# Performance work log

Measured on AMD Instinct MI355X. Metric: run time of the kernel, lower is better.

## Reference

```python
import jax, jax.numpy as jnp
import numpy as np

H = 2048       # hidden_size
NH = 16        # num_attention_heads
HN = H // NH   # per-head dim = 128
B = 2
S = 2048
ALPHA = 32.0   # cogview pb-relax alpha


def setup_inputs() -> dict:
    key = jax.random.key(0)
    k1, k2, k3 = jax.random.split(key, 3)
    hidden_states = jax.random.normal(k1, (B, S, H), dtype=jnp.float32)
    # causal lower-triangular float mask [1,1,s,s]
    ltor_mask = jnp.tril(jnp.ones((S, S), dtype=jnp.float32))[None, None]
    # fused QKV projection params (torch Linear: y = x @ W.T + b)
    lim_qkv = 1.0 / np.sqrt(H)
    W_qkv = jax.random.uniform(k2, (3 * H, H), jnp.float32, -lim_qkv, lim_qkv)
    b_qkv = jnp.zeros((3 * H,), jnp.float32)
    W_out = jax.random.uniform(k3, (H, H), jnp.float32, -lim_qkv, lim_qkv)
    b_out = jnp.zeros((H,), jnp.float32)
    return {"hidden_states": hidden_states, "ltor_mask": ltor_mask,
            "W_qkv": W_qkv, "b_qkv": b_qkv, "W_out": W_out, "b_out": b_out}


def reference(hidden_states, ltor_mask, W_qkv, b_qkv, W_out, b_out):
    b, s, h = hidden_states.shape
    # fused QKV projection: [b,s,3h]
    qkv = hidden_states @ W_qkv.T + b_qkv
    q, k, v = jnp.split(qkv, 3, axis=-1)
    # [b,s,h] -> [b,n,s,hn]
    def heads(t):
        return t.reshape(b, s, NH, HN).transpose(0, 2, 1, 3)
    q, k, v = heads(q), heads(k), heads(v)
    # cogview_pb_relax: scale query before matmul
    scores = jnp.einsum('bnqd,bnkd->bnqk', q / jnp.sqrt(jnp.float32(HN)), k)
    mask = ltor_mask[:, :, -scores.shape[-2]:]
    scores = scores * mask - 10000.0 * (1.0 - mask)
    # pb-relax max rescaling (max is detached)
    scaled = scores / ALPHA
    maxes = jax.lax.stop_gradient(jnp.max(scaled.reshape(b, NH, -1), axis=-1))
    scores = (scaled - maxes[:, :, None, None]) * ALPHA
    probs = jax.nn.softmax(scores, axis=-1)
    ctx = jnp.einsum('bnqk,bnkd->bnqd', probs, v)
    ctx = ctx.transpose(0, 2, 1, 3).reshape(b, s, h)
    out = ctx @ W_out.T + b_out
    return out
```

## Files before the change

kernel.cpp:

```cpp
#include <hip/hip_runtime.h>

typedef __bf16 bf16;
typedef bf16 bf16x4 __attribute__((ext_vector_type(4)));
typedef bf16 bf16x8 __attribute__((ext_vector_type(8)));
typedef float f32x4 __attribute__((ext_vector_type(4)));

#define Bb 2
#define Ss 2048
#define Hh 2048
#define NHh 16
#define HNd 128
#define H3 6144
#define Mm 4096
#define SCALE_QK 0.08838834764831843f

__device__ __forceinline__ void async_copy16(void* lds, const void* g) {
  __builtin_amdgcn_global_load_lds(
      (const __attribute__((address_space(1))) unsigned int*)g,
      (__attribute__((address_space(3))) unsigned int*)lds, 16, 0, 0);
}

__global__ __launch_bounds__(256) void cvt_kernel(const float* __restrict__ in,
                                                  bf16* __restrict__ out, int n) {
  int i = (blockIdx.x * 256 + threadIdx.x) * 4;
  if (i < n) {
    float4 v = *reinterpret_cast<const float4*>(in + i);
    bf16x4 o;
    o[0] = (bf16)v.x; o[1] = (bf16)v.y; o[2] = (bf16)v.z; o[3] = (bf16)v.w;
    *reinterpret_cast<bf16x4*>(out + i) = o;
  }
}

template <int QM, int QN, int NRD>
__device__ __forceinline__ void gemm_phase(
    const bf16* asb, const bf16* bsb, int lm, int lg, int wm, int wn,
    bf16x8 (&af)[4][2], bf16x8 (&bfr)[4][2]) {
  if (NRD & 2) {
#pragma unroll
    for (int mi = 0; mi < 4; ++mi)
#pragma unroll
      for (int kk = 0; kk < 2; ++kk) {
        const int row = wm * 128 + (QM * 4 + mi) * 16 + lm;
        af[mi][kk] = *reinterpret_cast<const bf16x8*>(
            (const char*)asb + row * 128 + ((kk * 64 + lg * 16) ^ ((lm & 7) << 4)));
      }
  }
  if (NRD & 1) {
#pragma unroll
    for (int nj = 0; nj < 2; ++nj)
#pragma unroll
      for (int kk = 0; kk < 2; ++kk) {
        const int row = wn * 64 + (QN * 2 + nj) * 16 + lm;
        bfr[QN * 2 + nj][kk] = *reinterpret_cast<const bf16x8*>(
            (const char*)bsb + row * 128 + ((kk * 64 + lg * 16) ^ ((lm & 7) << 4)));
      }
  }
}

template <int QM, int QN>
__device__ __forceinline__ void mfma_quad(const bf16x8 (&af)[4][2],
                                          const bf16x8 (&bfr)[4][2],
                                          f32x4 (&acc)[8][4]) {
#pragma unroll
  for (int kk = 0; kk < 2; ++kk)
#pragma unroll
    for (int mi = 0; mi < 4; ++mi)
#pragma unroll
      for (int nj = 0; nj < 2; ++nj)
        acc[QM * 4 + mi][QN * 2 + nj] = __builtin_amdgcn_mfma_f32_16x16x32_bf16(
            af[mi][kk], bfr[QN * 2 + nj][kk], acc[QM * 4 + mi][QN * 2 + nj], 0, 0, 0);
}

template <int OUT_F32>
__global__ __launch_bounds__(512, 2) void gemm256_kernel(
    const bf16* __restrict__ A, const bf16* __restrict__ Bw,
    const float* __restrict__ bias, void* __restrict__ Cout,
    int M, int N, int K) {
  __shared__ __align__(16) bf16 As[2][256 * 64];
  __shared__ __align__(16) bf16 Bs[2][256 * 64];

  const int tid = threadIdx.x;
  const int lane = tid & 63;
  const int w = tid >> 6;
  const int wm = w >> 2, wn = w & 3;
  const int lm = lane & 15, lg = lane >> 4;
  const int m0 = blockIdx.y * 256, n0 = blockIdx.x * 256;
  const int srow = lane >> 3;
  const int sslot = lane & 7;

  auto stage = [&](int b, int t) {
#pragma unroll
    for (int l = 0; l < 4; ++l) {
      const int r = l * 64 + w * 8 + srow;
      async_copy16(&As[b][l * 4096 + w * 512],
                   A + (size_t)(m0 + r) * K + t * 64 + (sslot ^ srow) * 8);
    }
#pragma unroll
    for (int l = 0; l < 4; ++l) {
      const int r = l * 64 + w * 8 + srow;
      async_copy16(&Bs[b][l * 4096 + w * 512],
                   Bw + (size_t)(n0 + r) * K + t * 64 + (sslot ^ srow) * 8);
    }
  };

  f32x4 acc[8][4] = {};
  bf16x8 af[4][2], bfr[4][2];

#define PHASE(BS, QM, QN, NRD, ST, VM)                                         \
  do {                                                                         \
    gemm_phase<QM, QN, NRD>(&As[BS][0], &Bs[BS][0], lm, lg, wm, wn, af, bfr);  \
    if ((ST) >= 0) stage((BS), (ST));                                          \
    __builtin_amdgcn_s_barrier();                                              \
    __builtin_amdgcn_s_setprio(1);                                             \
    mfma_quad<QM, QN>(af, bfr, acc);                                           \
    __builtin_amdgcn_s_setprio(0);                                             \
    if ((VM) == 8) asm volatile("s_waitcnt vmcnt(8)" ::: "memory");            \
    else if ((VM) == 0) asm volatile("s_waitcnt vmcnt(0)" ::: "memory");       \
    __builtin_amdgcn_s_barrier();                                              \
  } while (0)

  const int nt = K >> 6;
  stage(0, 0);
  stage(1, 1);
  asm volatile("s_waitcnt vmcnt(8)" ::: "memory");
  __builtin_amdgcn_s_barrier();

#pragma unroll 1
  for (int t = 0; t < nt - 2; t += 2) {
    PHASE(0, 0, 0, 3, -1, 9);
    PHASE(0, 0, 1, 1, -1, 9);
    PHASE(0, 1, 0, 2, -1, 9);
    PHASE(0, 1, 1, 0, t + 2, 8);
    PHASE(1, 0, 0, 3, -1, 9);
    PHASE(1, 0, 1, 1, -1, 9);
    PHASE(1, 1, 0, 2, -1, 9);
    PHASE(1, 1, 1, 0, t + 3, 8);
  }
  PHASE(0, 0, 0, 3, -1, 9);
  PHASE(0, 0, 1, 1, -1, 9);
  PHASE(0, 1, 0, 2, -1, 9);
  PHASE(0, 1, 1, 0, -1, 0);
  PHASE(1, 0, 0, 3, -1, 9);
  PHASE(1, 0, 1, 1, -1, 9);
  PHASE(1, 1, 0, 2, -1, 9);
  PHASE(1, 1, 1, 0, -1, 9);
#undef PHASE

#pragma unroll
  for (int mi = 0; mi < 8; ++mi) {
#pragma unroll
    for (int nj = 0; nj < 4; ++nj) {
      const int col = n0 + wn * 64 + nj * 16 + lm;
      const float bv = bias[col];
      const int r0 = m0 + wm * 128 + mi * 16 + lg * 4;
#pragma unroll
      for (int r = 0; r < 4; ++r) {
        const float v = acc[mi][nj][r] + bv;
        if (OUT_F32)
          reinterpret_cast<float*>(Cout)[(size_t)(r0 + r) * N + col] = v;
        else
          reinterpret_cast<bf16*>(Cout)[(size_t)(r0 + r) * N + col] = (bf16)v;
      }
    }
  }
}

template <int OUT_F32>
__global__ __launch_bounds__(256) void gemm_bt_kernel(
    const bf16* __restrict__ A, const bf16* __restrict__ Bw,
    const float* __restrict__ bias, void* __restrict__ Cout,
    int M, int N, int K) {
  __shared__ __align__(16) bf16 As[128][64];
  __shared__ __align__(16) bf16 Bs[128][64];

  const int tid = threadIdx.x;
  const int lane = tid & 63;
  const int w = tid >> 6;
  const int wr = w >> 1, wc = w & 1;
  const int m0 = blockIdx.y * 128;
  const int n0 = blockIdx.x * 128;
  const int srow = lane >> 3;
  const int sslot = lane & 7;

  f32x4 acc[4][4] = {};

  for (int k0 = 0; k0 < K; k0 += 64) {
#pragma unroll
    for (int c = 0; c < 4; ++c) {
      const int ci = c * 4 + w;
      const int row = ci * 8 + srow;
      async_copy16((char*)&As[0][0] + ci * 1024,
                   A + (size_t)(m0 + row) * K + k0 + sslot * 8);
      async_copy16((char*)&Bs[0][0] + ci * 1024,
                   Bw + (size_t)(n0 + row) * K + k0 + sslot * 8);
    }
    __syncthreads();

#pragma unroll
    for (int kk = 0; kk < 2; ++kk) {
      const int kc = kk * 32 + (lane >> 4) * 8;
      bf16x8 af[4], bfr[4];
#pragma unroll
      for (int mi = 0; mi < 4; ++mi)
        af[mi] = *reinterpret_cast<const bf16x8*>(&As[wr * 64 + mi * 16 + (lane & 15)][kc]);
#pragma unroll
      for (int nj = 0; nj < 4; ++nj)
        bfr[nj] = *reinterpret_cast<const bf16x8*>(&Bs[wc * 64 + nj * 16 + (lane & 15)][kc]);
#pragma unroll
      for (int mi = 0; mi < 4; ++mi)
#pragma unroll
        for (int nj = 0; nj < 4; ++nj)
          acc[mi][nj] = __builtin_amdgcn_mfma_f32_16x16x32_bf16(af[mi], bfr[nj], acc[mi][nj], 0, 0, 0);
    }
    __syncthreads();
  }

#pragma unroll
  for (int mi = 0; mi < 4; ++mi) {
#pragma unroll
    for (int nj = 0; nj < 4; ++nj) {
      const int col = n0 + wc * 64 + nj * 16 + (lane & 15);
      const float bv = bias[col];
      const int r0 = m0 + wr * 64 + mi * 16 + (lane >> 4) * 4;
#pragma unroll
      for (int r = 0; r < 4; ++r) {
        const float v = acc[mi][nj][r] + bv;
        if (OUT_F32)
          reinterpret_cast<float*>(Cout)[(size_t)(r0 + r) * N + col] = v;
        else
          reinterpret_cast<bf16*>(Cout)[(size_t)(r0 + r) * N + col] = (bf16)v;
      }
    }
  }
}

__device__ __forceinline__ void attn_tile(
    const char* ksb, const char* vtb, bf16* psw,
    const bf16x8* qf, f32x4* acc, float* mrow, float* lrow,
    int qr0, int kv0, bool diag, int lm, int lg) {
  float p[4][4];
#pragma unroll
  for (int kt = 0; kt < 4; ++kt) {
    f32x4 s = {};
    const int r = kt * 16 + lm;
#pragma unroll
    for (int kk = 0; kk < 4; ++kk) {
      bf16x8 kf = *reinterpret_cast<const bf16x8*>(
          ksb + r * 256 + ((kk * 64 + lg * 16) ^ ((lm & 7) << 4)));
      s = __builtin_amdgcn_mfma_f32_16x16x32_bf16(qf[kk], kf, s, 0, 0, 0);
    }
    if (diag) {
      const int col = kv0 + kt * 16 + lm;
#pragma unroll
      for (int rr = 0; rr < 4; ++rr)
        p[kt][rr] = (col <= qr0 + lg * 4 + rr) ? s[rr] * SCALE_QK : -3.0e38f;
    } else {
#pragma unroll
      for (int rr = 0; rr < 4; ++rr) p[kt][rr] = s[rr] * SCALE_QK;
    }
  }
#pragma unroll
  for (int rr = 0; rr < 4; ++rr) {
    float pm = fmaxf(fmaxf(p[0][rr], p[1][rr]), fmaxf(p[2][rr], p[3][rr]));
#pragma unroll
    for (int off = 1; off < 16; off <<= 1) pm = fmaxf(pm, __shfl_xor(pm, off));
    const float mnew = fmaxf(mrow[rr], pm);
    const float sc = __expf(mrow[rr] - mnew);
    mrow[rr] = mnew;
    float sum = 0.f;
#pragma unroll
    for (int kt = 0; kt < 4; ++kt) { p[kt][rr] = __expf(p[kt][rr] - mnew); sum += p[kt][rr]; }
#pragma unroll
    for (int off = 1; off < 16; off <<= 1) sum += __shfl_xor(sum, off);
    lrow[rr] = lrow[rr] * sc + sum;
#pragma unroll
    for (int dt = 0; dt < 8; ++dt) acc[dt][rr] *= sc;
  }
#pragma unroll
  for (int kt = 0; kt < 4; ++kt)
#pragma unroll
    for (int rr = 0; rr < 4; ++rr)
      psw[(lg * 4 + rr) * 72 + kt * 16 + lm] = (bf16)p[kt][rr];
  __syncthreads();
#pragma unroll
  for (int kb = 0; kb < 2; ++kb) {
    bf16x8 pa = *reinterpret_cast<const bf16x8*>(&psw[lm * 72 + kb * 32 + lg * 8]);
#pragma unroll
    for (int dt = 0; dt < 8; ++dt) {
      const int d = dt * 16 + lm;
      bf16x8 vf = *reinterpret_cast<const bf16x8*>(
          vtb + d * 128 + ((kb * 64 + lg * 16) ^ (((dt * 2 + (lm >> 3)) & 7) << 4)));
      acc[dt] = __builtin_amdgcn_mfma_f32_16x16x32_bf16(pa, vf, acc[dt], 0, 0, 0);
    }
  }
}

__global__ __launch_bounds__(256, 2) void attn_kernel(const bf16* __restrict__ qkv,
                                                      bf16* __restrict__ ctx) {
  __shared__ __align__(16) bf16 Ks[64 * 128];
  __shared__ __align__(16) bf16 Vt[128 * 64];
  __shared__ __align__(16) bf16 Ps[4 * 16 * 72];

  const int tid = threadIdx.x;
  const int lane = tid & 63;
  const int w = tid >> 6;
  const int lm = lane & 15;
  const int lg = lane >> 4;
  const int pr = blockIdx.x;
  const int bh = blockIdx.y;
  const int b = bh >> 4;
  const int h = bh & 15;
  const int qtA = 31 - pr;
  const int qtB = pr;

  const size_t rs = H3;
  const bf16* qbase = qkv + (size_t)b * Ss * rs + (size_t)h * HNd;
  const bf16* kbase = qbase + Hh;
  const bf16* vbase = qbase + 2 * Hh;

  const int qrA = qtA * 64 + w * 16;
  const int qrB = qtB * 64 + w * 16;

  bf16x8 qfA[4], qfB[4];
#pragma unroll
  for (int kk = 0; kk < 4; ++kk) {
    qfA[kk] = *reinterpret_cast<const bf16x8*>(qbase + (size_t)(qrA + lm) * rs + kk * 32 + lg * 8);
    qfB[kk] = *reinterpret_cast<const bf16x8*>(qbase + (size_t)(qrB + lm) * rs + kk * 32 + lg * 8);
  }

  f32x4 accA[8] = {}, accB[8] = {};
  float mA[4], lA[4], mB[4], lB[4];
#pragma unroll
  for (int r = 0; r < 4; ++r) { mA[r] = mB[r] = -3.0e38f; lA[r] = lB[r] = 0.f; }

  char* ksb = (char*)Ks;
  char* vtb = (char*)Vt;
  bf16* psw = Ps + w * 16 * 72;

  const int nkv = qtA + 1;
  for (int t = 0; t < nkv; ++t) {
    const int kv0 = t * 64;
#pragma unroll
    for (int c = 0; c < 4; ++c) {
      const int ci = c * 4 + w;
      const int row = ci * 4 + lg;
      async_copy16(ksb + ci * 1024,
                   kbase + (size_t)(kv0 + row) * rs + (lm ^ (row & 7)) * 8);
    }
#pragma unroll
    for (int j = 0; j < 4; ++j) {
      const int idx = j * 256 + tid;
      const int kv = idx >> 4;
      const int d8 = idx & 15;
      bf16x8 v = *reinterpret_cast<const bf16x8*>(vbase + (size_t)(kv0 + kv) * rs + d8 * 8);
#pragma unroll
      for (int e = 0; e < 8; ++e)
        *reinterpret_cast<bf16*>(vtb + (d8 * 8 + e) * 128 + ((kv * 2) ^ ((d8 & 7) << 4))) = v[e];
    }
    __syncthreads();

    attn_tile(ksb, vtb, psw, qfA, accA, mA, lA, qrA, kv0, t == qtA, lm, lg);
    if (t <= qtB)
      attn_tile(ksb, vtb, psw, qfB, accB, mB, lB, qrB, kv0, t == qtB, lm, lg);
    __syncthreads();
  }

  bf16* cbase = ctx + (size_t)b * Ss * Hh + (size_t)h * HNd;
#pragma unroll
  for (int dt = 0; dt < 8; ++dt)
#pragma unroll
    for (int r = 0; r < 4; ++r) {
      cbase[(size_t)(qrA + lg * 4 + r) * Hh + dt * 16 + lm] = (bf16)(accA[dt][r] / lA[r]);
      cbase[(size_t)(qrB + lg * 4 + r) * Hh + dt * 16 + lm] = (bf16)(accB[dt][r] / lB[r]);
    }
}

extern "C" void kernel_launch(void* const* d_in, const int* in_sizes, int n_in,
                              void* d_out, int out_size, void* d_ws, size_t ws_size,
                              hipStream_t stream) {
  const float* hidden = (const float*)d_in[0];
  const float* Wqkv = (const float*)d_in[2];
  const float* bqkv = (const float*)d_in[3];
  const float* Wout = (const float*)d_in[4];
  const float* bout = (const float*)d_in[5];
  float* out = (float*)d_out;

  char* ws = (char*)d_ws;
  bf16* hid_bf = (bf16*)ws;  ws += (size_t)Mm * Hh * 2;
  bf16* wqkv_bf = (bf16*)ws; ws += (size_t)H3 * Hh * 2;
  bf16* wout_bf = (bf16*)ws; ws += (size_t)Hh * Hh * 2;
  bf16* qkv_bf = (bf16*)ws;  ws += (size_t)Mm * H3 * 2;
  bf16* ctx_bf = (bf16*)ws;  ws += (size_t)Mm * Hh * 2;

  cvt_kernel<<<(Mm * Hh / 4 + 255) / 256, 256, 0, stream>>>(hidden, hid_bf, Mm * Hh);
  cvt_kernel<<<(H3 * Hh / 4 + 255) / 256, 256, 0, stream>>>(Wqkv, wqkv_bf, H3 * Hh);
  cvt_kernel<<<(Hh * Hh / 4 + 255) / 256, 256, 0, stream>>>(Wout, wout_bf, Hh * Hh);

  gemm256_kernel<0><<<dim3(H3 / 256, Mm / 256), 512, 0, stream>>>(
      hid_bf, wqkv_bf, bqkv, qkv_bf, Mm, H3, Hh);
  attn_kernel<<<dim3(16, Bb * NHh), 256, 0, stream>>>(qkv_bf, ctx_bf);
  gemm_bt_kernel<1><<<dim3(Hh / 128, Mm / 128), 256, 0, stream>>>(
      ctx_bf, wout_bf, bout, out, Mm, Hh, Hh);
}
```

Measured before the change: 319.4 us.

## Switch QKV GEMM to 256x192 tiles with XCD-aware block remapping

Reworks the QKV projection GEMM from 256x256 to 256x192 output tiles, which gives a 32x16 grid of 512 blocks instead of 24x16 = 384 and so fills the CUs more evenly. Each wave now computes 128x48, reading its B fragments once per k-step and A fragments in four 2-row phases. The A and B async copies are staged separately at different phases to spread out memory traffic. Blocks are also remapped so that groups of adjacent column tiles land on the same XCD, which should improve L2 reuse. Less reuse per tile and a more intricate vmcnt schedule carry some risk to correctness and to latency hiding.

```diff
diff --git a/kernel.cpp b/kernel.cpp
--- a/kernel.cpp
+++ b/kernel.cpp
@@ -31,126 +31,136 @@
   }
 }
 
-template <int QM, int QN, int NRD>
-__device__ __forceinline__ void gemm_phase(
-    const bf16* asb, const bf16* bsb, int lm, int lg, int wm, int wn,
-    bf16x8 (&af)[4][2], bf16x8 (&bfr)[4][2]) {
-  if (NRD & 2) {
-#pragma unroll
-    for (int mi = 0; mi < 4; ++mi)
+
+struct G192Frags {
+  bf16x8 af[2][2];
+  bf16x8 bfr[3][2];
+};
+
+template <int MP, int RDB>
+__device__ __forceinline__ void g192_reads(const bf16* asb, const bf16* bsb,
+                                           int lm, int lg, int wm, int wn,
+                                           G192Frags& f) {
+  if (RDB) {
+#pragma unroll
+    for (int nj = 0; nj < 3; ++nj)
 #pragma unroll
       for (int kk = 0; kk < 2; ++kk) {
-        const int row = wm * 128 + (QM * 4 + mi) * 16 + lm;
-        af[mi][kk] = *reinterpret_cast<const bf16x8*>(
-            (const char*)asb + row * 128 + ((kk * 64 + lg * 16) ^ ((lm & 7) << 4)));
-      }
-  }
-  if (NRD & 1) {
-#pragma unroll
-    for (int nj = 0; nj < 2; ++nj)
-#pragma unroll
-      for (int kk = 0; kk < 2; ++kk) {
-        const int row = wn * 64 + (QN * 2 + nj) * 16 + lm;
-        bfr[QN * 2 + nj][kk] = *reinterpret_cast<const bf16x8*>(
+        const int row = wn * 48 + nj * 16 + lm;
+        f.bfr[nj][kk] = *reinterpret_cast<const bf16x8*>(
             (const char*)bsb + row * 128 + ((kk * 64 + lg * 16) ^ ((lm & 7) << 4)));
       }
   }
-}
-
-template <int QM, int QN>
-__device__ __forceinline__ void mfma_quad(const bf16x8 (&af)[4][2],
-                                          const bf16x8 (&bfr)[4][2],
-                                          f32x4 (&acc)[8][4]) {
+#pragma unroll
+  for (int i = 0; i < 2; ++i)
+#pragma unroll
+    for (int kk = 0; kk < 2; ++kk) {
+      const int row = wm * 128 + (MP * 2 + i) * 16 + lm;
+      f.af[i][kk] = *reinterpret_cast<const bf16x8*>(
+          (const char*)asb + row * 128 + ((kk * 64 + lg * 16) ^ ((lm & 7) << 4)));
+    }
+}
+
+template <int MP>
+__device__ __forceinline__ void g192_mfma(const G192Frags& f, f32x4 (&acc)[8][3]) {
 #pragma unroll
   for (int kk = 0; kk < 2; ++kk)
 #pragma unroll
-    for (int mi = 0; mi < 4; ++mi)
-#pragma unroll
-      for (int nj = 0; nj < 2; ++nj)
-        acc[QM * 4 + mi][QN * 2 + nj] = __builtin_amdgcn_mfma_f32_16x16x32_bf16(
-            af[mi][kk], bfr[QN * 2 + nj][kk], acc[QM * 4 + mi][QN * 2 + nj], 0, 0, 0);
+    for (int i = 0; i < 2; ++i)
+#pragma unroll
+      for (int nj = 0; nj < 3; ++nj)
+        acc[MP * 2 + i][nj] = __builtin_amdgcn_mfma_f32_16x16x32_bf16(
+            f.af[i][kk], f.bfr[nj][kk], acc[MP * 2 + i][nj], 0, 0, 0);
 }
 
 template <int OUT_F32>
-__global__ __launch_bounds__(512, 2) void gemm256_kernel(
+__global__ __launch_bounds__(512, 2) void gemm192_kernel(
     const bf16* __restrict__ A, const bf16* __restrict__ Bw,
     const float* __restrict__ bias, void* __restrict__ Cout,
     int M, int N, int K) {
   __shared__ __align__(16) bf16 As[2][256 * 64];
-  __shared__ __align__(16) bf16 Bs[2][256 * 64];
+  __shared__ __align__(16) bf16 Bs[2][192 * 64];
 
   const int tid = threadIdx.x;
   const int lane = tid & 63;
   const int w = tid >> 6;
   const int wm = w >> 2, wn = w & 3;
   const int lm = lane & 15, lg = lane >> 4;
-  const int m0 = blockIdx.y * 256, n0 = blockIdx.x * 256;
   const int srow = lane >> 3;
   const int sslot = lane & 7;
 
-  auto stage = [&](int b, int t) {
+  const int id = blockIdx.y * gridDim.x + blockIdx.x;
+  const int xcd = id & 7, rem = id >> 3;
+  const int bx = xcd * 4 + (rem & 3);
+  const int by = rem >> 2;
+  const int m0 = by * 256, n0 = bx * 192;
+
+  auto stageA = [&](int b, int t) {
 #pragma unroll
     for (int l = 0; l < 4; ++l) {
       const int r = l * 64 + w * 8 + srow;
-      async_copy16(&As[b][l * 4096 + w * 512],
+      async_copy16((char*)&As[b][0] + l * 8192 + w * 1024,
                    A + (size_t)(m0 + r) * K + t * 64 + (sslot ^ srow) * 8);
     }
-#pragma unroll
-    for (int l = 0; l < 4; ++l) {
+  };
+  auto stageB = [&](int b, int t) {
+#pragma unroll
+    for (int l = 0; l < 3; ++l) {
       const int r = l * 64 + w * 8 + srow;
-      async_copy16(&Bs[b][l * 4096 + w * 512],
+      async_copy16((char*)&Bs[b][0] + l * 8192 + w * 1024,
                    Bw + (size_t)(n0 + r) * K + t * 64 + (sslot ^ srow) * 8);
     }
   };
 
-  f32x4 acc[8][4] = {};
-  bf16x8 af[4][2], bfr[4][2];
-
-#define PHASE(BS, QM, QN, NRD, ST, VM)                                         \
+  f32x4 acc[8][3] = {};
+  G192Frags f;
+
+#define PHASE(BS, MP, RDB, VM, ...)                                            \
   do {                                                                         \
-    gemm_phase<QM, QN, NRD>(&As[BS][0], &Bs[BS][0], lm, lg, wm, wn, af, bfr);  \
-    if ((ST) >= 0) stage((BS), (ST));                                          \
+    g192_reads<MP, RDB>(&As[BS][0], &Bs[BS][0], lm, lg, wm, wn, f);            \
+    __VA_ARGS__;                                                               \
     __builtin_amdgcn_s_barrier();                                              \
     __builtin_amdgcn_s_setprio(1);                                             \
-    mfma_quad<QM, QN>(af, bfr, acc);                                           \
+    g192_mfma<MP>(f, acc);                                                     \
     __builtin_amdgcn_s_setprio(0);                                             \
-    if ((VM) == 8) asm volatile("s_waitcnt vmcnt(8)" ::: "memory");            \
+    if ((VM) == 3) asm volatile("s_waitcnt vmcnt(3)" ::: "memory");            \
     else if ((VM) == 0) asm volatile("s_waitcnt vmcnt(0)" ::: "memory");       \
     __builtin_amdgcn_s_barrier();                                              \
   } while (0)
 
   const int nt = K >> 6;
-  stage(0, 0);
-  stage(1, 1);
-  asm volatile("s_waitcnt vmcnt(8)" ::: "memory");
+  stageB(0, 0);
+  stageA(0, 0);
+  stageB(1, 1);
+  asm volatile("s_waitcnt vmcnt(3)" ::: "memory");
   __builtin_amdgcn_s_barrier();
 
 #pragma unroll 1
   for (int t = 0; t < nt - 2; t += 2) {
-    PHASE(0, 0, 0, 3, -1, 9);
-    PHASE(0, 0, 1, 1, -1, 9);
-    PHASE(0, 1, 0, 2, -1, 9);
-    PHASE(0, 1, 1, 0, t + 2, 8);
-    PHASE(1, 0, 0, 3, -1, 9);
-    PHASE(1, 0, 1, 1, -1, 9);
-    PHASE(1, 1, 0, 2, -1, 9);
-    PHASE(1, 1, 1, 0, t + 3, 8);
-  }
-  PHASE(0, 0, 0, 3, -1, 9);
-  PHASE(0, 0, 1, 1, -1, 9);
-  PHASE(0, 1, 0, 2, -1, 9);
-  PHASE(0, 1, 1, 0, -1, 0);
-  PHASE(1, 0, 0, 3, -1, 9);
-  PHASE(1, 0, 1, 1, -1, 9);
-  PHASE(1, 1, 0, 2, -1, 9);
-  PHASE(1, 1, 1, 0, -1, 9);
+    PHASE(0, 0, 1, 9, stageA(1, t + 1));
+    PHASE(0, 1, 0, 9, stageB(0, t + 2));
+    PHASE(0, 2, 0, 9, );
+    PHASE(0, 3, 0, 3, );
+    PHASE(1, 0, 1, 9, stageA(0, t + 2));
+    PHASE(1, 1, 0, 9, stageB(1, t + 3));
+    PHASE(1, 2, 0, 9, );
+    PHASE(1, 3, 0, 3, );
+  }
+  PHASE(0, 0, 1, 9, stageA(1, nt - 1));
+  PHASE(0, 1, 0, 9, );
+  PHASE(0, 2, 0, 9, );
+  PHASE(0, 3, 0, 0, );
+  PHASE(1, 0, 1, 9, );
+  PHASE(1, 1, 0, 9, );
+  PHASE(1, 2, 0, 9, );
+  PHASE(1, 3, 0, 9, );
 #undef PHASE
 
 #pragma unroll
   for (int mi = 0; mi < 8; ++mi) {
 #pragma unroll
-    for (int nj = 0; nj < 4; ++nj) {
-      const int col = n0 + wn * 64 + nj * 16 + lm;
+    for (int nj = 0; nj < 3; ++nj) {
+      const int col = n0 + wn * 48 + nj * 16 + lm;
       const float bv = bias[col];
       const int r0 = m0 + wm * 128 + mi * 16 + lg * 4;
 #pragma unroll
@@ -396,7 +406,7 @@
   cvt_kernel<<<(H3 * Hh / 4 + 255) / 256, 256, 0, stream>>>(Wqkv, wqkv_bf, H3 * Hh);
   cvt_kernel<<<(Hh * Hh / 4 + 255) / 256, 256, 0, stream>>>(Wout, wout_bf, Hh * Hh);
 
-  gemm256_kernel<0><<<dim3(H3 / 256, Mm / 256), 512, 0, stream>>>(
+  gemm192_kernel<0><<<dim3(H3 / 192, Mm / 256), 512, 0, stream>>>(
       hid_bf, wqkv_bf, bqkv, qkv_bf, Mm, H3, Hh);
   attn_kernel<<<dim3(16, Bb * NHh), 256, 0, stream>>>(qkv_bf, ctx_bf);
   gemm_bt_kernel<1><<<dim3(Hh / 128, Mm / 128), 256, 0, stream>>>(
```

After: 299.4 us. -6.3%, faster.
